# Performance work log

Measured on AMD Instinct MI355X. Metric: run time of the kernel, lower is better.

## Reference

```python
import jax, jax.numpy as jnp
import numpy as np

B, T1, H, P, V = 4096, 65, 64, 50, 32
D = H + P  # input_size = 114


def setup_inputs() -> dict:
    key = jax.random.key(0)
    ks = jax.random.split(key, 20)
    s = 1.0 / np.sqrt(D)
    sh = 1.0 / np.sqrt(H)
    inp = {
        "phonetic_input": jax.random.normal(ks[0], (B, P), dtype=jnp.float32),
        "char_seq": jax.random.randint(ks[1], (B, T1), 0, V, dtype=jnp.int64),
        "emb": jax.random.normal(ks[2], (V, H), dtype=jnp.float32).at[0].set(0.0),  # padding_idx=0
        "W_rx": jax.random.uniform(ks[3], (D, H), jnp.float32, -s, s),
        "b_rx": jax.random.uniform(ks[4], (H,), jnp.float32, -s, s),
        "W_rh": jax.random.uniform(ks[5], (H, H), jnp.float32, -sh, sh),
        "b_rh": jax.random.uniform(ks[6], (H,), jnp.float32, -sh, sh),
        "W_zx": jax.random.uniform(ks[7], (D, H), jnp.float32, -s, s),
        "b_zx": jax.random.uniform(ks[8], (H,), jnp.float32, -s, s),
        "W_zh": jax.random.uniform(ks[9], (H, H), jnp.float32, -sh, sh),
        "b_zh": jax.random.uniform(ks[10], (H,), jnp.float32, -sh, sh),
        "W_hx": jax.random.uniform(ks[11], (D, H), jnp.float32, -s, s),
        "b_hx": jax.random.uniform(ks[12], (H,), jnp.float32, -s, s),
        "W_hh": jax.random.uniform(ks[13], (H, H), jnp.float32, -sh, sh),
        "b_hh": jax.random.uniform(ks[14], (H,), jnp.float32, -sh, sh),
        "W_proj": jax.random.uniform(ks[15], (H, V), jnp.float32, -sh, sh),
        "b_proj": jax.random.uniform(ks[16], (V,), jnp.float32, -sh, sh),
    }
    return inp


def reference(phonetic_input, char_seq, emb, W_rx, b_rx, W_rh, b_rh, W_zx, b_zx,
              W_zh, b_zh, W_hx, b_hx, W_hh, b_hh, W_proj, b_proj):
    input_seq = char_seq[:, :-1]          # [B, T]
    target_seq = char_seq[:, 1:]          # [B, T]
    Bsz, T = input_seq.shape

    char_emb = emb[input_seq]                                   # [B, T, H]
    phon = jnp.broadcast_to(phonetic_input[:, None, :], (Bsz, T, P))
    x = jnp.concatenate([char_emb, phon], axis=2)               # [B, T, D]

    # Hoist input-side projections into batched GEMMs, [T, B, H] for scan
    xr = jnp.einsum('btd,dh->tbh', x, W_rx) + b_rx
    xz = jnp.einsum('btd,dh->tbh', x, W_zx) + b_zx
    xh = jnp.einsum('btd,dh->tbh', x, W_hx) + b_hx

    h0 = jnp.zeros((Bsz, H), dtype=x.dtype)

    def step(h, inputs):
        xr_t, xz_t, xh_t = inputs
        r = jax.nn.sigmoid(xr_t + h @ W_rh + b_rh)
        z = jax.nn.sigmoid(xz_t + h @ W_zh + b_zh)
        c = jnp.tanh(xh_t + (r * h) @ W_hh + b_hh)
        h_new = (1.0 - z) * h + z * c
        return h_new, h_new

    _, hs = jax.lax.scan(step, h0, (xr, xz, xh))                # [T, B, H]
    logits = jnp.einsum('tbh,hv->btv', hs, W_proj) + b_proj     # [B, T, V]

    # cross_entropy with ignore_index=0 (mean over non-ignored)
    targets = target_seq.reshape(-1)
    logp = jax.nn.log_softmax(logits.reshape(-1, V), axis=-1)
    nll = -jnp.take_along_axis(logp, targets[:, None], axis=-1)[:, 0]
    mask = (targets != 0).astype(logits.dtype)
    loss = jnp.sum(nll * mask) / jnp.maximum(jnp.sum(mask), 1.0)
    return logits, loss
```

## Files before the change

kernel.cpp:

```cpp
#include <hip/hip_runtime.h>
#include <stdint.h>

#define Bsz 4096
#define Tn  64
#define T1n 65
#define Hn  64
#define Pn  50
#define Vn  32

typedef __attribute__((ext_vector_type(8))) short short8;
typedef __attribute__((ext_vector_type(4))) float floatx4;

__device__ __forceinline__ float bf2f(unsigned short u) {
  union { unsigned int i; float f; } x; x.i = ((unsigned int)u) << 16; return x.f;
}
__device__ __forceinline__ unsigned short f2bf(float f) {
  union { float f; unsigned int i; } x; x.f = f;
  return (unsigned short)((x.i + 0x7FFFu + ((x.i >> 16) & 1u)) >> 16);
}

__device__ __forceinline__ short8 load_bfrag(const float* __restrict__ W, int ncols, int col, int kbase) {
  short8 f;
#pragma unroll
  for (int j = 0; j < 8; ++j) f[j] = (short)f2bf(W[(long)(kbase + j) * ncols + col]);
  return f;
}

__launch_bounds__(256)
__global__ void gru_kernel(const float* __restrict__ phon,
                           const int* __restrict__ cs,
                           const float* __restrict__ emb,
                           const float* __restrict__ Wrx, const float* __restrict__ brx,
                           const float* __restrict__ Wrh, const float* __restrict__ brh,
                           const float* __restrict__ Wzx, const float* __restrict__ bzx,
                           const float* __restrict__ Wzh, const float* __restrict__ bzh,
                           const float* __restrict__ Whx, const float* __restrict__ bhx,
                           const float* __restrict__ Whh, const float* __restrict__ bhh,
                           const float* __restrict__ Wpj, const float* __restrict__ bpj_g,
                           float* __restrict__ ws,
                           float* __restrict__ outp) {
  __shared__ unsigned short tbl_s[3 * 32 * 66];
  __shared__ __align__(16) unsigned short hist_s[16 * 1152];
  __shared__ __align__(16) unsigned short rh_s[16 * 72];
  __shared__ unsigned char code_s[16 * 68];
  __shared__ unsigned short emb_s[32 * 64];
  __shared__ unsigned short ph_s[16 * 52];
  __shared__ int det_s[1];
  __shared__ float red_s[8];

  const int tid = threadIdx.x;
  const int b0 = blockIdx.x * 16;
  const int w = tid >> 6, lane = tid & 63, q = lane >> 4, c16 = lane & 15;
  const int jcol = w * 16 + c16;

  if (tid == 0) det_s[0] = 0;
  __syncthreads();
  if (tid < 128 && cs[2 * tid + 1] != 0) atomicOr(&det_s[0], 1);
  __syncthreads();
  const bool is64 = (det_s[0] == 0);

  for (int i = tid; i < 16 * 72; i += 256) hist_s[15 * 1152 + i] = 0;
  for (int i = tid; i < 32 * 64; i += 256) emb_s[i] = f2bf(emb[i]);
  for (int i = tid; i < 16 * Pn; i += 256) {
    int m = i / Pn, p = i - m * Pn;
    ph_s[m * 52 + p] = f2bf(phon[(long)(b0 + m) * Pn + p]);
  }
  for (int i = tid; i < 16 * T1n; i += 256) {
    int m = i / T1n, t = i - m * T1n;
    long idx = (long)(b0 + m) * T1n + t;
    int c = is64 ? cs[2 * idx] : cs[idx];
    code_s[m * 68 + t] = (unsigned char)c;
  }

  short8 Brh0 = load_bfrag(Wrh, Hn, jcol, q * 8);
  short8 Brh1 = load_bfrag(Wrh, Hn, jcol, 32 + q * 8);
  short8 Bzh0 = load_bfrag(Wzh, Hn, jcol, q * 8);
  short8 Bzh1 = load_bfrag(Wzh, Hn, jcol, 32 + q * 8);
  short8 Bhh0 = load_bfrag(Whh, Hn, jcol, q * 8);
  short8 Bhh1 = load_bfrag(Whh, Hn, jcol, 32 + q * 8);
  short8 Bp00 = load_bfrag(Wpj, Vn, c16,      q * 8);
  short8 Bp01 = load_bfrag(Wpj, Vn, c16,      32 + q * 8);
  short8 Bp10 = load_bfrag(Wpj, Vn, 16 + c16, q * 8);
  short8 Bp11 = load_bfrag(Wpj, Vn, 16 + c16, 32 + q * 8);
  const float bpj0 = bpj_g[c16], bpj1 = bpj_g[16 + c16];

  __syncthreads();

  for (int g = 0; g < 3; ++g) {
    const float* W  = (g == 0) ? Wrx : (g == 1) ? Wzx : Whx;
    const float* bx = (g == 0) ? brx : (g == 1) ? bzx : bhx;
    const float* bh = (g == 0) ? brh : (g == 1) ? bzh : bhh;
    float acc[8] = {0.f, 0.f, 0.f, 0.f, 0.f, 0.f, 0.f, 0.f};
    float bias = bx[lane] + bh[lane];
    for (int d = 0; d < Hn; ++d) {
      float wv = W[(long)d * Hn + lane];
#pragma unroll
      for (int k = 0; k < 8; ++k)
        acc[k] += bf2f(emb_s[(w + 4 * k) * Hn + d]) * wv;
    }
#pragma unroll
    for (int k = 0; k < 8; ++k)
      tbl_s[g * 2112 + (w + 4 * k) * 66 + lane] = f2bf(acc[k] + bias);
  }

  float ph_r[4] = {0.f, 0.f, 0.f, 0.f};
  float ph_z[4] = {0.f, 0.f, 0.f, 0.f};
  float ph_h[4] = {0.f, 0.f, 0.f, 0.f};
  for (int p = 0; p < Pn; ++p) {
    float wr = Wrx[(long)(Hn + p) * Hn + jcol];
    float wz = Wzx[(long)(Hn + p) * Hn + jcol];
    float wh = Whx[(long)(Hn + p) * Hn + jcol];
#pragma unroll
    for (int r = 0; r < 4; ++r) {
      float xv = bf2f(ph_s[(q * 4 + r) * 52 + p]);
      ph_r[r] += xv * wr; ph_z[r] += xv * wz; ph_h[r] += xv * wh;
    }
  }

  float h[4] = {0.f, 0.f, 0.f, 0.f};
  float nll_acc = 0.f, cnt_acc = 0.f;

  __syncthreads();

  for (int qi = 0; qi < 4; ++qi) {
    for (int tt = 0; tt < 16; ++tt) {
      const int t = qi * 16 + tt;
      int cr[4];
#pragma unroll
      for (int r = 0; r < 4; ++r) cr[r] = code_s[(q * 4 + r) * 68 + t];

      const unsigned short* hp = &hist_s[((tt + 15) & 15) * 1152];
      short8 a0 = *(const short8*)&hp[c16 * 72 + q * 8];
      short8 a1 = *(const short8*)&hp[c16 * 72 + 32 + q * 8];
      floatx4 accr = {0.f, 0.f, 0.f, 0.f}, accz = {0.f, 0.f, 0.f, 0.f};
      accr = __builtin_amdgcn_mfma_f32_16x16x32_bf16(a0, Brh0, accr, 0, 0, 0);
      accr = __builtin_amdgcn_mfma_f32_16x16x32_bf16(a1, Brh1, accr, 0, 0, 0);
      accz = __builtin_amdgcn_mfma_f32_16x16x32_bf16(a0, Bzh0, accz, 0, 0, 0);
      accz = __builtin_amdgcn_mfma_f32_16x16x32_bf16(a1, Bzh1, accz, 0, 0, 0);
      float z[4];
#pragma unroll
      for (int r = 0; r < 4; ++r) {
        float xr = bf2f(tbl_s[0 * 2112 + cr[r] * 66 + jcol]) + ph_r[r] + accr[r];
        float rr = 1.f / (1.f + __expf(-xr));
        float xz = bf2f(tbl_s[1 * 2112 + cr[r] * 66 + jcol]) + ph_z[r] + accz[r];
        z[r] = 1.f / (1.f + __expf(-xz));
        rh_s[(q * 4 + r) * 72 + jcol] = f2bf(rr * h[r]);
      }
      __syncthreads();

      short8 p0 = *(const short8*)&rh_s[c16 * 72 + q * 8];
      short8 p1 = *(const short8*)&rh_s[c16 * 72 + 32 + q * 8];
      floatx4 accc = {0.f, 0.f, 0.f, 0.f};
      accc = __builtin_amdgcn_mfma_f32_16x16x32_bf16(p0, Bhh0, accc, 0, 0, 0);
      accc = __builtin_amdgcn_mfma_f32_16x16x32_bf16(p1, Bhh1, accc, 0, 0, 0);
      unsigned short* hw = &hist_s[tt * 1152];
#pragma unroll
      for (int r = 0; r < 4; ++r) {
        float xh = bf2f(tbl_s[2 * 2112 + cr[r] * 66 + jcol]) + ph_h[r] + accc[r];
        float e = __expf(2.f * xh);
        float c = 1.f - 2.f / (e + 1.f);
        float hn = (1.f - z[r]) * h[r] + z[r] * c;
        h[r] = hn;
        hw[(q * 4 + r) * 72 + jcol] = f2bf(hn);
      }
      __syncthreads();
    }

    for (int k = 0; k < 4; ++k) {
      const int tt = k * 4 + w;
      const int t = qi * 16 + tt;
      const unsigned short* hp = &hist_s[tt * 1152];
      const short8 ha0 = *(const short8*)&hp[c16 * 72 + q * 8];
      const short8 ha1 = *(const short8*)&hp[c16 * 72 + 32 + q * 8];
      floatx4 l0 = {0.f, 0.f, 0.f, 0.f}, l1 = {0.f, 0.f, 0.f, 0.f};
      l0 = __builtin_amdgcn_mfma_f32_16x16x32_bf16(ha0, Bp00, l0, 0, 0, 0);
      l0 = __builtin_amdgcn_mfma_f32_16x16x32_bf16(ha1, Bp01, l0, 0, 0, 0);
      l1 = __builtin_amdgcn_mfma_f32_16x16x32_bf16(ha0, Bp10, l1, 0, 0, 0);
      l1 = __builtin_amdgcn_mfma_f32_16x16x32_bf16(ha1, Bp11, l1, 0, 0, 0);
#pragma unroll
      for (int r = 0; r < 4; ++r) {
        float lg0 = l0[r] + bpj0, lg1 = l1[r] + bpj1;
        float mx = fmaxf(lg0, lg1);
#pragma unroll
        for (int off = 8; off >= 1; off >>= 1) mx = fmaxf(mx, __shfl_xor(mx, off));
        float s = __expf(lg0 - mx) + __expf(lg1 - mx);
#pragma unroll
        for (int off = 8; off >= 1; off >>= 1) s += __shfl_xor(s, off);
        float lse = mx + __logf(s);
        int m = q * 4 + r;
        long base = (((long)(b0 + m)) * Tn + t) * Vn;
        outp[base + c16] = lg0;
        outp[base + 16 + c16] = lg1;
        int targ = code_s[m * 68 + t + 1];
        if (targ != 0 && c16 == (targ & 15)) {
          float lt = (targ >> 4) ? lg1 : lg0;
          nll_acc += lse - lt; cnt_acc += 1.f;
        }
      }
    }
    __syncthreads();
  }

#pragma unroll
  for (int off = 32; off >= 1; off >>= 1) {
    nll_acc += __shfl_xor(nll_acc, off);
    cnt_acc += __shfl_xor(cnt_acc, off);
  }
  if (lane == 0) { red_s[w] = nll_acc; red_s[4 + w] = cnt_acc; }
  __syncthreads();
  if (tid == 0) {
    ws[2 * blockIdx.x]     = red_s[0] + red_s[1] + red_s[2] + red_s[3];
    ws[2 * blockIdx.x + 1] = red_s[4] + red_s[5] + red_s[6] + red_s[7];
  }
}

__global__ void loss_kernel(const float* __restrict__ ws, float* __restrict__ outp) {
  int lane = threadIdx.x;
  float n = 0.f, c = 0.f;
  for (int i = lane; i < 256; i += 64) { n += ws[2 * i]; c += ws[2 * i + 1]; }
#pragma unroll
  for (int off = 32; off >= 1; off >>= 1) {
    n += __shfl_xor(n, off);
    c += __shfl_xor(c, off);
  }
  if (lane == 0) outp[(size_t)Bsz * Tn * Vn] = n / fmaxf(c, 1.f);
}

extern "C" void kernel_launch(void* const* d_in, const int* in_sizes, int n_in,
                              void* d_out, int out_size, void* d_ws, size_t ws_size,
                              hipStream_t stream) {
  const float* phon = (const float*)d_in[0];
  const int*   cs   = (const int*)d_in[1];
  const float* emb  = (const float*)d_in[2];
  const float* Wrx  = (const float*)d_in[3];
  const float* brx  = (const float*)d_in[4];
  const float* Wrh  = (const float*)d_in[5];
  const float* brh  = (const float*)d_in[6];
  const float* Wzx  = (const float*)d_in[7];
  const float* bzx  = (const float*)d_in[8];
  const float* Wzh  = (const float*)d_in[9];
  const float* bzh  = (const float*)d_in[10];
  const float* Whx  = (const float*)d_in[11];
  const float* bhx  = (const float*)d_in[12];
  const float* Whh  = (const float*)d_in[13];
  const float* bhh  = (const float*)d_in[14];
  const float* Wpj  = (const float*)d_in[15];
  const float* bpj  = (const float*)d_in[16];
  float* ws = (float*)d_ws;

  hipLaunchKernelGGL(gru_kernel, dim3(Bsz / 16), dim3(256), 0, stream,
                     phon, cs, emb, Wrx, brx, Wrh, brh, Wzx, bzx, Wzh, bzh,
                     Whx, bhx, Whh, bhh, Wpj, bpj, ws, (float*)d_out);
  hipLaunchKernelGGL(loss_kernel, dim3(1), dim3(64), 0, stream, ws, (float*)d_out);
}
```

Baseline: 189.4 us.

## Split GRU scan and output projection into separate kernels via in-place bf16 history

Moves the per-timestep output projection, log-softmax and NLL out of the sequential recurrent kernel into a separate highly parallel kernel with one block per batch row. The scan kernel now only writes its bf16 hidden-state history to global memory, reusing the logits output buffer in place; each row's history occupies the same bytes its logits later overwrite. This shortens the serial critical path of the scan, which launches only one 256-thread block per 16 batch rows. The cost is an extra global write and read of the history. It also packs the character codes four per word, uses hardware reciprocal for sigmoid and tanh, and accumulates the loss with atomics after a zeroing kernel.

New measurement: 280.2 us. 47.9% more time.

```diff
diff --git a/kernel.cpp b/kernel.cpp
--- a/kernel.cpp
+++ b/kernel.cpp
@@ -18,6 +18,12 @@
   union { float f; unsigned int i; } x; x.f = f;
   return (unsigned short)((x.i + 0x7FFFu + ((x.i >> 16) & 1u)) >> 16);
 }
+__device__ __forceinline__ float fast_sigmoid(float x) {
+  return __builtin_amdgcn_rcpf(1.f + __expf(-x));
+}
+__device__ __forceinline__ float fast_tanh(float x) {
+  return 1.f - 2.f * __builtin_amdgcn_rcpf(1.f + __expf(2.f * x));
+}
 
 __device__ __forceinline__ short8 load_bfrag(const float* __restrict__ W, int ncols, int col, int kbase) {
   short8 f;
@@ -26,27 +32,28 @@
   return f;
 }
 
+__global__ void zero_kernel(float* __restrict__ ws) {
+  if (threadIdx.x < 2) ws[threadIdx.x] = 0.f;
+}
+
 __launch_bounds__(256)
-__global__ void gru_kernel(const float* __restrict__ phon,
-                           const int* __restrict__ cs,
-                           const float* __restrict__ emb,
-                           const float* __restrict__ Wrx, const float* __restrict__ brx,
-                           const float* __restrict__ Wrh, const float* __restrict__ brh,
-                           const float* __restrict__ Wzx, const float* __restrict__ bzx,
-                           const float* __restrict__ Wzh, const float* __restrict__ bzh,
-                           const float* __restrict__ Whx, const float* __restrict__ bhx,
-                           const float* __restrict__ Whh, const float* __restrict__ bhh,
-                           const float* __restrict__ Wpj, const float* __restrict__ bpj_g,
-                           float* __restrict__ ws,
-                           float* __restrict__ outp) {
+__global__ void gru_scan(const float* __restrict__ phon,
+                         const int* __restrict__ cs,
+                         const float* __restrict__ emb,
+                         const float* __restrict__ Wrx, const float* __restrict__ brx,
+                         const float* __restrict__ Wrh, const float* __restrict__ brh,
+                         const float* __restrict__ Wzx, const float* __restrict__ bzx,
+                         const float* __restrict__ Wzh, const float* __restrict__ bzh,
+                         const float* __restrict__ Whx, const float* __restrict__ bhx,
+                         const float* __restrict__ Whh, const float* __restrict__ bhh,
+                         unsigned short* __restrict__ histg) {
   __shared__ unsigned short tbl_s[3 * 32 * 66];
   __shared__ __align__(16) unsigned short hist_s[16 * 1152];
   __shared__ __align__(16) unsigned short rh_s[16 * 72];
-  __shared__ unsigned char code_s[16 * 68];
+  __shared__ unsigned int code4_s[64 * 4];
   __shared__ unsigned short emb_s[32 * 64];
   __shared__ unsigned short ph_s[16 * 52];
   __shared__ int det_s[1];
-  __shared__ float red_s[8];
 
   const int tid = threadIdx.x;
   const int b0 = blockIdx.x * 16;
@@ -65,11 +72,16 @@
     int m = i / Pn, p = i - m * Pn;
     ph_s[m * 52 + p] = f2bf(phon[(long)(b0 + m) * Pn + p]);
   }
-  for (int i = tid; i < 16 * T1n; i += 256) {
-    int m = i / T1n, t = i - m * T1n;
-    long idx = (long)(b0 + m) * T1n + t;
-    int c = is64 ? cs[2 * idx] : cs[idx];
-    code_s[m * 68 + t] = (unsigned char)c;
+  {
+    int t = tid >> 2, qq = tid & 3;
+    unsigned int pk = 0;
+#pragma unroll
+    for (int r = 0; r < 4; ++r) {
+      long idx = (long)(b0 + qq * 4 + r) * T1n + t;
+      int c = is64 ? cs[2 * idx] : cs[idx];
+      pk |= ((unsigned int)(c & 255)) << (8 * r);
+    }
+    code4_s[t * 4 + qq] = pk;
   }
 
   short8 Brh0 = load_bfrag(Wrh, Hn, jcol, q * 8);
@@ -78,11 +90,6 @@
   short8 Bzh1 = load_bfrag(Wzh, Hn, jcol, 32 + q * 8);
   short8 Bhh0 = load_bfrag(Whh, Hn, jcol, q * 8);
   short8 Bhh1 = load_bfrag(Whh, Hn, jcol, 32 + q * 8);
-  short8 Bp00 = load_bfrag(Wpj, Vn, c16,      q * 8);
-  short8 Bp01 = load_bfrag(Wpj, Vn, c16,      32 + q * 8);
-  short8 Bp10 = load_bfrag(Wpj, Vn, 16 + c16, q * 8);
-  short8 Bp11 = load_bfrag(Wpj, Vn, 16 + c16, 32 + q * 8);
-  const float bpj0 = bpj_g[c16], bpj1 = bpj_g[16 + c16];
 
   __syncthreads();
 
@@ -118,16 +125,13 @@
   }
 
   float h[4] = {0.f, 0.f, 0.f, 0.f};
-  float nll_acc = 0.f, cnt_acc = 0.f;
 
   __syncthreads();
 
   for (int qi = 0; qi < 4; ++qi) {
     for (int tt = 0; tt < 16; ++tt) {
       const int t = qi * 16 + tt;
-      int cr[4];
-#pragma unroll
-      for (int r = 0; r < 4; ++r) cr[r] = code_s[(q * 4 + r) * 68 + t];
+      unsigned int pk = code4_s[t * 4 + q];
 
       const unsigned short* hp = &hist_s[((tt + 15) & 15) * 1152];
       short8 a0 = *(const short8*)&hp[c16 * 72 + q * 8];
@@ -140,10 +144,11 @@
       float z[4];
 #pragma unroll
       for (int r = 0; r < 4; ++r) {
-        float xr = bf2f(tbl_s[0 * 2112 + cr[r] * 66 + jcol]) + ph_r[r] + accr[r];
-        float rr = 1.f / (1.f + __expf(-xr));
-        float xz = bf2f(tbl_s[1 * 2112 + cr[r] * 66 + jcol]) + ph_z[r] + accz[r];
-        z[r] = 1.f / (1.f + __expf(-xz));
+        int cr = (pk >> (8 * r)) & 255;
+        float xr = bf2f(tbl_s[0 * 2112 + cr * 66 + jcol]) + ph_r[r] + accr[r];
+        float rr = fast_sigmoid(xr);
+        float xz = bf2f(tbl_s[1 * 2112 + cr * 66 + jcol]) + ph_z[r] + accz[r];
+        z[r] = fast_sigmoid(xz);
         rh_s[(q * 4 + r) * 72 + jcol] = f2bf(rr * h[r]);
       }
       __syncthreads();
@@ -156,9 +161,9 @@
       unsigned short* hw = &hist_s[tt * 1152];
 #pragma unroll
       for (int r = 0; r < 4; ++r) {
-        float xh = bf2f(tbl_s[2 * 2112 + cr[r] * 66 + jcol]) + ph_h[r] + accc[r];
-        float e = __expf(2.f * xh);
-        float c = 1.f - 2.f / (e + 1.f);
+        int cr = (pk >> (8 * r)) & 255;
+        float xh = bf2f(tbl_s[2 * 2112 + cr * 66 + jcol]) + ph_h[r] + accc[r];
+        float c = fast_tanh(xh);
         float hn = (1.f - z[r]) * h[r] + z[r] * c;
         h[r] = hn;
         hw[(q * 4 + r) * 72 + jcol] = f2bf(hn);
@@ -166,39 +171,76 @@
       __syncthreads();
     }
 
-    for (int k = 0; k < 4; ++k) {
-      const int tt = k * 4 + w;
-      const int t = qi * 16 + tt;
-      const unsigned short* hp = &hist_s[tt * 1152];
-      const short8 ha0 = *(const short8*)&hp[c16 * 72 + q * 8];
-      const short8 ha1 = *(const short8*)&hp[c16 * 72 + 32 + q * 8];
-      floatx4 l0 = {0.f, 0.f, 0.f, 0.f}, l1 = {0.f, 0.f, 0.f, 0.f};
-      l0 = __builtin_amdgcn_mfma_f32_16x16x32_bf16(ha0, Bp00, l0, 0, 0, 0);
-      l0 = __builtin_amdgcn_mfma_f32_16x16x32_bf16(ha1, Bp01, l0, 0, 0, 0);
-      l1 = __builtin_amdgcn_mfma_f32_16x16x32_bf16(ha0, Bp10, l1, 0, 0, 0);
-      l1 = __builtin_amdgcn_mfma_f32_16x16x32_bf16(ha1, Bp11, l1, 0, 0, 0);
-#pragma unroll
-      for (int r = 0; r < 4; ++r) {
-        float lg0 = l0[r] + bpj0, lg1 = l1[r] + bpj1;
-        float mx = fmaxf(lg0, lg1);
-#pragma unroll
-        for (int off = 8; off >= 1; off >>= 1) mx = fmaxf(mx, __shfl_xor(mx, off));
-        float s = __expf(lg0 - mx) + __expf(lg1 - mx);
-#pragma unroll
-        for (int off = 8; off >= 1; off >>= 1) s += __shfl_xor(s, off);
-        float lse = mx + __logf(s);
-        int m = q * 4 + r;
-        long base = (((long)(b0 + m)) * Tn + t) * Vn;
-        outp[base + c16] = lg0;
-        outp[base + 16 + c16] = lg1;
-        int targ = code_s[m * 68 + t + 1];
-        if (targ != 0 && c16 == (targ & 15)) {
-          float lt = (targ >> 4) ? lg1 : lg0;
-          nll_acc += lse - lt; cnt_acc += 1.f;
-        }
-      }
-    }
-    __syncthreads();
+    for (int u = tid; u < 2048; u += 256) {
+      int slot = u >> 7, rem = u & 127;
+      int m = rem >> 3, grp = rem & 7;
+      short8 v = *(const short8*)&hist_s[slot * 1152 + m * 72 + grp * 8];
+      *(short8*)&histg[(((long)(b0 + m)) * Tn + qi * 16 + slot) * Hn + grp * 8] = v;
+    }
+  }
+}
+
+__launch_bounds__(256)
+__global__ void proj_kernel(const int* __restrict__ cs,
+                            const float* __restrict__ Wpj, const float* __restrict__ bpj_g,
+                            float* __restrict__ ws,
+                            float* __restrict__ outp) {
+  __shared__ unsigned char targ_s[64];
+  __shared__ int det_s[1];
+  __shared__ float red_s[8];
+
+  const int tid = threadIdx.x;
+  const long b = blockIdx.x;
+  const int w = tid >> 6, lane = tid & 63, q = lane >> 4, c16 = lane & 15;
+  const unsigned short* hist = (const unsigned short*)outp;
+
+  if (tid == 0) det_s[0] = 0;
+  __syncthreads();
+  if (tid < 128 && cs[2 * tid + 1] != 0) atomicOr(&det_s[0], 1);
+  __syncthreads();
+  const bool is64 = (det_s[0] == 0);
+  if (tid < 64) {
+    long idx = b * T1n + tid + 1;
+    targ_s[tid] = (unsigned char)(is64 ? cs[2 * idx] : cs[idx]);
+  }
+
+  short8 Bp00 = load_bfrag(Wpj, Vn, c16,      q * 8);
+  short8 Bp01 = load_bfrag(Wpj, Vn, c16,      32 + q * 8);
+  short8 Bp10 = load_bfrag(Wpj, Vn, 16 + c16, q * 8);
+  short8 Bp11 = load_bfrag(Wpj, Vn, 16 + c16, 32 + q * 8);
+  const float bpj0 = bpj_g[c16], bpj1 = bpj_g[16 + c16];
+  __syncthreads();
+
+  const long cell0 = b * Tn + w * 16;
+  const short8 ha0 = *(const short8*)&hist[(cell0 + c16) * Hn + q * 8];
+  const short8 ha1 = *(const short8*)&hist[(cell0 + c16) * Hn + 32 + q * 8];
+  floatx4 l0 = {0.f, 0.f, 0.f, 0.f}, l1 = {0.f, 0.f, 0.f, 0.f};
+  l0 = __builtin_amdgcn_mfma_f32_16x16x32_bf16(ha0, Bp00, l0, 0, 0, 0);
+  l0 = __builtin_amdgcn_mfma_f32_16x16x32_bf16(ha1, Bp01, l0, 0, 0, 0);
+  l1 = __builtin_amdgcn_mfma_f32_16x16x32_bf16(ha0, Bp10, l1, 0, 0, 0);
+  l1 = __builtin_amdgcn_mfma_f32_16x16x32_bf16(ha1, Bp11, l1, 0, 0, 0);
+
+  float nll_acc = 0.f, cnt_acc = 0.f;
+#pragma unroll
+  for (int r = 0; r < 4; ++r) {
+    int m = q * 4 + r;
+    int t = w * 16 + m;
+    float lg0 = l0[r] + bpj0, lg1 = l1[r] + bpj1;
+    float mx = fmaxf(lg0, lg1);
+#pragma unroll
+    for (int off = 8; off >= 1; off >>= 1) mx = fmaxf(mx, __shfl_xor(mx, off));
+    float s = __expf(lg0 - mx) + __expf(lg1 - mx);
+#pragma unroll
+    for (int off = 8; off >= 1; off >>= 1) s += __shfl_xor(s, off);
+    float lse = mx + __logf(s);
+    long base = (b * Tn + t) * Vn;
+    outp[base + c16] = lg0;
+    outp[base + 16 + c16] = lg1;
+    int targ = targ_s[t];
+    if (targ != 0 && c16 == (targ & 15)) {
+      float lt = (targ >> 4) ? lg1 : lg0;
+      nll_acc += lse - lt; cnt_acc += 1.f;
+    }
   }
 
 #pragma unroll
@@ -209,21 +251,14 @@
   if (lane == 0) { red_s[w] = nll_acc; red_s[4 + w] = cnt_acc; }
   __syncthreads();
   if (tid == 0) {
-    ws[2 * blockIdx.x]     = red_s[0] + red_s[1] + red_s[2] + red_s[3];
-    ws[2 * blockIdx.x + 1] = red_s[4] + red_s[5] + red_s[6] + red_s[7];
+    atomicAdd(&ws[0], red_s[0] + red_s[1] + red_s[2] + red_s[3]);
+    atomicAdd(&ws[1], red_s[4] + red_s[5] + red_s[6] + red_s[7]);
   }
 }
 
 __global__ void loss_kernel(const float* __restrict__ ws, float* __restrict__ outp) {
-  int lane = threadIdx.x;
-  float n = 0.f, c = 0.f;
-  for (int i = lane; i < 256; i += 64) { n += ws[2 * i]; c += ws[2 * i + 1]; }
-#pragma unroll
-  for (int off = 32; off >= 1; off >>= 1) {
-    n += __shfl_xor(n, off);
-    c += __shfl_xor(c, off);
-  }
-  if (lane == 0) outp[(size_t)Bsz * Tn * Vn] = n / fmaxf(c, 1.f);
+  if (threadIdx.x == 0)
+    outp[(size_t)Bsz * Tn * Vn] = ws[0] / fmaxf(ws[1], 1.f);
 }
 
 extern "C" void kernel_launch(void* const* d_in, const int* in_sizes, int n_in,
@@ -248,8 +283,11 @@
   const float* bpj  = (const float*)d_in[16];
   float* ws = (float*)d_ws;
 
-  hipLaunchKernelGGL(gru_kernel, dim3(Bsz / 16), dim3(256), 0, stream,
+  hipLaunchKernelGGL(zero_kernel, dim3(1), dim3(64), 0, stream, ws);
+  hipLaunchKernelGGL(gru_scan, dim3(Bsz / 16), dim3(256), 0, stream,
                      phon, cs, emb, Wrx, brx, Wrh, brh, Wzx, bzx, Wzh, bzh,
-                     Whx, bhx, Whh, bhh, Wpj, bpj, ws, (float*)d_out);
+                     Whx, bhx, Whh, bhh, (unsigned short*)d_out);
+  hipLaunchKernelGGL(proj_kernel, dim3(Bsz), dim3(256), 0, stream,
+                     cs, Wpj, bpj, ws, (float*)d_out);
   hipLaunchKernelGGL(loss_kernel, dim3(1), dim3(64), 0, stream, ws, (float*)d_out);
 }
```

## Run each 16-row GRU batch tile in a single wavefront with permuted hidden layout

Applied to the files above, without the earlier changes.

Each block now holds one 64-lane wavefront instead of four, and each lane computes all four 16-column hidden tiles. To make this work, the K dimension of the recurrent weights is permuted so the MFMA output layout can be written back as packed short4 rows. The embedding and phonetic input projections now use MFMA, codes are packed four per word, and sigmoid/tanh use hardware reciprocal. The log-softmax drops the max subtraction. The aim is cheaper block-wide barriers and less per-step overhead, at the cost of 4x more MFMA work per wave, only 256 waves in flight, and possible overflow in the softmax without the max shift.

After: 280.5 us. 1.48x slower.

```diff
diff --git a/kernel.cpp b/kernel.cpp
--- a/kernel.cpp
+++ b/kernel.cpp
@@ -9,6 +9,7 @@
 #define Vn  32
 
 typedef __attribute__((ext_vector_type(8))) short short8;
+typedef __attribute__((ext_vector_type(4))) short short4v;
 typedef __attribute__((ext_vector_type(4))) float floatx4;
 
 __device__ __forceinline__ float bf2f(unsigned short u) {
@@ -18,183 +19,248 @@
   union { float f; unsigned int i; } x; x.f = f;
   return (unsigned short)((x.i + 0x7FFFu + ((x.i >> 16) & 1u)) >> 16);
 }
-
-__device__ __forceinline__ short8 load_bfrag(const float* __restrict__ W, int ncols, int col, int kbase) {
+__device__ __forceinline__ float fast_sigmoid(float x) {
+  return __builtin_amdgcn_rcpf(1.f + __expf(-x));
+}
+__device__ __forceinline__ float fast_tanh(float x) {
+  return 1.f - 2.f * __builtin_amdgcn_rcpf(1.f + __expf(2.f * x));
+}
+
+__device__ __forceinline__ short8 load_bfrag_pi(const float* __restrict__ W, int ncols, int col, int kbase) {
   short8 f;
 #pragma unroll
-  for (int j = 0; j < 8; ++j) f[j] = (short)f2bf(W[(long)(kbase + j) * ncols + col]);
+  for (int j = 0; j < 8; ++j) {
+    int k = kbase + j;
+    int p = ((k & 3) << 4) | (k >> 2);
+    f[j] = (short)f2bf(W[(long)p * ncols + col]);
+  }
   return f;
 }
 
-__launch_bounds__(256)
-__global__ void gru_kernel(const float* __restrict__ phon,
-                           const int* __restrict__ cs,
-                           const float* __restrict__ emb,
-                           const float* __restrict__ Wrx, const float* __restrict__ brx,
-                           const float* __restrict__ Wrh, const float* __restrict__ brh,
-                           const float* __restrict__ Wzx, const float* __restrict__ bzx,
-                           const float* __restrict__ Wzh, const float* __restrict__ bzh,
-                           const float* __restrict__ Whx, const float* __restrict__ bhx,
-                           const float* __restrict__ Whh, const float* __restrict__ bhh,
-                           const float* __restrict__ Wpj, const float* __restrict__ bpj_g,
-                           float* __restrict__ ws,
-                           float* __restrict__ outp) {
-  __shared__ unsigned short tbl_s[3 * 32 * 66];
+__launch_bounds__(64, 1)
+__global__ void gru_all(const float* __restrict__ phon,
+                        const int* __restrict__ cs,
+                        const float* __restrict__ emb,
+                        const float* __restrict__ Wrx, const float* __restrict__ brx,
+                        const float* __restrict__ Wrh, const float* __restrict__ brh,
+                        const float* __restrict__ Wzx, const float* __restrict__ bzx,
+                        const float* __restrict__ Wzh, const float* __restrict__ bzh,
+                        const float* __restrict__ Whx, const float* __restrict__ bhx,
+                        const float* __restrict__ Whh, const float* __restrict__ bhh,
+                        const float* __restrict__ Wpj, const float* __restrict__ bpj_g,
+                        float* __restrict__ ws,
+                        float* __restrict__ outp) {
   __shared__ __align__(16) unsigned short hist_s[16 * 1152];
-  __shared__ __align__(16) unsigned short rh_s[16 * 72];
-  __shared__ unsigned char code_s[16 * 68];
-  __shared__ unsigned short emb_s[32 * 64];
-  __shared__ unsigned short ph_s[16 * 52];
-  __shared__ int det_s[1];
-  __shared__ float red_s[8];
-
-  const int tid = threadIdx.x;
+  __shared__ __align__(16) unsigned short rh_s[1152];
+  __shared__ __align__(16) unsigned short tblT_s[3 * 2176];
+  __shared__ unsigned int code4_s[T1n * 4];
+
+  const int lane = threadIdx.x;
+  const int q = lane >> 4, c16 = lane & 15;
   const int b0 = blockIdx.x * 16;
-  const int w = tid >> 6, lane = tid & 63, q = lane >> 4, c16 = lane & 15;
-  const int jcol = w * 16 + c16;
-
-  if (tid == 0) det_s[0] = 0;
-  __syncthreads();
-  if (tid < 128 && cs[2 * tid + 1] != 0) atomicOr(&det_s[0], 1);
-  __syncthreads();
-  const bool is64 = (det_s[0] == 0);
-
-  for (int i = tid; i < 16 * 72; i += 256) hist_s[15 * 1152 + i] = 0;
-  for (int i = tid; i < 32 * 64; i += 256) emb_s[i] = f2bf(emb[i]);
-  for (int i = tid; i < 16 * Pn; i += 256) {
-    int m = i / Pn, p = i - m * Pn;
-    ph_s[m * 52 + p] = f2bf(phon[(long)(b0 + m) * Pn + p]);
-  }
-  for (int i = tid; i < 16 * T1n; i += 256) {
-    int m = i / T1n, t = i - m * T1n;
-    long idx = (long)(b0 + m) * T1n + t;
-    int c = is64 ? cs[2 * idx] : cs[idx];
-    code_s[m * 68 + t] = (unsigned char)c;
-  }
-
-  short8 Brh0 = load_bfrag(Wrh, Hn, jcol, q * 8);
-  short8 Brh1 = load_bfrag(Wrh, Hn, jcol, 32 + q * 8);
-  short8 Bzh0 = load_bfrag(Wzh, Hn, jcol, q * 8);
-  short8 Bzh1 = load_bfrag(Wzh, Hn, jcol, 32 + q * 8);
-  short8 Bhh0 = load_bfrag(Whh, Hn, jcol, q * 8);
-  short8 Bhh1 = load_bfrag(Whh, Hn, jcol, 32 + q * 8);
-  short8 Bp00 = load_bfrag(Wpj, Vn, c16,      q * 8);
-  short8 Bp01 = load_bfrag(Wpj, Vn, c16,      32 + q * 8);
-  short8 Bp10 = load_bfrag(Wpj, Vn, 16 + c16, q * 8);
-  short8 Bp11 = load_bfrag(Wpj, Vn, 16 + c16, 32 + q * 8);
+  const floatx4 zf = {0.f, 0.f, 0.f, 0.f};
+
+  const bool is64 = (__ballot(cs[2 * lane + 1] != 0) == 0ull);
+
+#pragma unroll
+  for (int kk = 0; kk < 5; ++kk) {
+    int idx = lane + 64 * kk;
+    if (idx < T1n * 4) {
+      int t = idx >> 2, qq = idx & 3;
+      unsigned int pk = 0;
+#pragma unroll
+      for (int r = 0; r < 4; ++r) {
+        long id = (long)(b0 + qq * 4 + r) * T1n + t;
+        int c = is64 ? cs[2 * id] : cs[id];
+        pk |= ((unsigned int)(c & 255)) << (8 * r);
+      }
+      code4_s[idx] = pk;
+    }
+  }
+  for (int i = lane; i < 1152; i += 64) hist_s[15 * 1152 + i] = 0;
+
+  short8 Brh[4][2], Bzh[4][2], Bhh[4][2], Bpj[2][2];
+#pragma unroll
+  for (int T = 0; T < 4; ++T)
+#pragma unroll
+    for (int hh = 0; hh < 2; ++hh) {
+      Brh[T][hh] = load_bfrag_pi(Wrh, Hn, T * 16 + c16, hh * 32 + q * 8);
+      Bzh[T][hh] = load_bfrag_pi(Wzh, Hn, T * 16 + c16, hh * 32 + q * 8);
+      Bhh[T][hh] = load_bfrag_pi(Whh, Hn, T * 16 + c16, hh * 32 + q * 8);
+    }
+#pragma unroll
+  for (int vt = 0; vt < 2; ++vt)
+#pragma unroll
+    for (int hh = 0; hh < 2; ++hh)
+      Bpj[vt][hh] = load_bfrag_pi(Wpj, Vn, vt * 16 + c16, hh * 32 + q * 8);
   const float bpj0 = bpj_g[c16], bpj1 = bpj_g[16 + c16];
-
-  __syncthreads();
 
   for (int g = 0; g < 3; ++g) {
     const float* W  = (g == 0) ? Wrx : (g == 1) ? Wzx : Whx;
     const float* bx = (g == 0) ? brx : (g == 1) ? bzx : bhx;
     const float* bh = (g == 0) ? brh : (g == 1) ? bzh : bhh;
-    float acc[8] = {0.f, 0.f, 0.f, 0.f, 0.f, 0.f, 0.f, 0.f};
-    float bias = bx[lane] + bh[lane];
-    for (int d = 0; d < Hn; ++d) {
-      float wv = W[(long)d * Hn + lane];
-#pragma unroll
-      for (int k = 0; k < 8; ++k)
-        acc[k] += bf2f(emb_s[(w + 4 * k) * Hn + d]) * wv;
-    }
-#pragma unroll
-    for (int k = 0; k < 8; ++k)
-      tbl_s[g * 2112 + (w + 4 * k) * 66 + lane] = f2bf(acc[k] + bias);
-  }
-
-  float ph_r[4] = {0.f, 0.f, 0.f, 0.f};
-  float ph_z[4] = {0.f, 0.f, 0.f, 0.f};
-  float ph_h[4] = {0.f, 0.f, 0.f, 0.f};
-  for (int p = 0; p < Pn; ++p) {
-    float wr = Wrx[(long)(Hn + p) * Hn + jcol];
-    float wz = Wzx[(long)(Hn + p) * Hn + jcol];
-    float wh = Whx[(long)(Hn + p) * Hn + jcol];
-#pragma unroll
-    for (int r = 0; r < 4; ++r) {
-      float xv = bf2f(ph_s[(q * 4 + r) * 52 + p]);
-      ph_r[r] += xv * wr; ph_z[r] += xv * wz; ph_h[r] += xv * wh;
-    }
-  }
-
-  float h[4] = {0.f, 0.f, 0.f, 0.f};
-  float nll_acc = 0.f, cnt_acc = 0.f;
-
+    short8 Bx[4][2];
+#pragma unroll
+    for (int T = 0; T < 4; ++T)
+#pragma unroll
+      for (int hh = 0; hh < 2; ++hh) {
+        short8 f;
+#pragma unroll
+        for (int j = 0; j < 8; ++j)
+          f[j] = (short)f2bf(W[(long)(hh * 32 + q * 8 + j) * Hn + T * 16 + c16]);
+        Bx[T][hh] = f;
+      }
+    float bias[4];
+#pragma unroll
+    for (int T = 0; T < 4; ++T) bias[T] = bx[T * 16 + c16] + bh[T * 16 + c16];
+    for (int mt = 0; mt < 2; ++mt) {
+      short8 A0, A1;
+#pragma unroll
+      for (int j = 0; j < 8; ++j) {
+        A0[j] = (short)f2bf(emb[(long)(mt * 16 + c16) * Hn + q * 8 + j]);
+        A1[j] = (short)f2bf(emb[(long)(mt * 16 + c16) * Hn + 32 + q * 8 + j]);
+      }
+      floatx4 acc[4];
+#pragma unroll
+      for (int T = 0; T < 4; ++T) {
+        acc[T] = __builtin_amdgcn_mfma_f32_16x16x32_bf16(A0, Bx[T][0], zf, 0, 0, 0);
+        acc[T] = __builtin_amdgcn_mfma_f32_16x16x32_bf16(A1, Bx[T][1], acc[T], 0, 0, 0);
+      }
+#pragma unroll
+      for (int r = 0; r < 4; ++r) {
+        short4v tv;
+#pragma unroll
+        for (int T = 0; T < 4; ++T) tv[T] = (short)f2bf(acc[T][r] + bias[T]);
+        int v = mt * 16 + q * 4 + r;
+        *(short4v*)&tblT_s[g * 2176 + v * 68 + c16 * 4] = tv;
+      }
+    }
+  }
+
+  floatx4 ph_r[4], ph_z[4], ph_h[4];
+  {
+    short8 Ap0, Ap1;
+#pragma unroll
+    for (int j = 0; j < 8; ++j) {
+      int k0 = q * 8 + j;
+      Ap0[j] = (short)f2bf(phon[(long)(b0 + c16) * Pn + k0]);
+      int k1 = 32 + q * 8 + j;
+      Ap1[j] = (k1 < Pn) ? (short)f2bf(phon[(long)(b0 + c16) * Pn + k1]) : (short)0;
+    }
+    for (int g = 0; g < 3; ++g) {
+      const float* W = (g == 0) ? Wrx : (g == 1) ? Wzx : Whx;
+      short8 Bp[4][2];
+#pragma unroll
+      for (int T = 0; T < 4; ++T)
+#pragma unroll
+        for (int hh = 0; hh < 2; ++hh) {
+          short8 f;
+#pragma unroll
+          for (int j = 0; j < 8; ++j) {
+            int k = hh * 32 + q * 8 + j;
+            f[j] = (k < Pn) ? (short)f2bf(W[(long)(Hn + k) * Hn + T * 16 + c16]) : (short)0;
+          }
+          Bp[T][hh] = f;
+        }
+#pragma unroll
+      for (int T = 0; T < 4; ++T) {
+        floatx4 acc = __builtin_amdgcn_mfma_f32_16x16x32_bf16(Ap0, Bp[T][0], zf, 0, 0, 0);
+        acc = __builtin_amdgcn_mfma_f32_16x16x32_bf16(Ap1, Bp[T][1], acc, 0, 0, 0);
+        if (g == 0) ph_r[T] = acc; else if (g == 1) ph_z[T] = acc; else ph_h[T] = acc;
+      }
+    }
+  }
+
+  floatx4 h4[4] = {zf, zf, zf, zf};
+  float nll = 0.f, cnt = 0.f;
   __syncthreads();
 
   for (int qi = 0; qi < 4; ++qi) {
     for (int tt = 0; tt < 16; ++tt) {
       const int t = qi * 16 + tt;
-      int cr[4];
-#pragma unroll
-      for (int r = 0; r < 4; ++r) cr[r] = code_s[(q * 4 + r) * 68 + t];
-
       const unsigned short* hp = &hist_s[((tt + 15) & 15) * 1152];
       short8 a0 = *(const short8*)&hp[c16 * 72 + q * 8];
       short8 a1 = *(const short8*)&hp[c16 * 72 + 32 + q * 8];
-      floatx4 accr = {0.f, 0.f, 0.f, 0.f}, accz = {0.f, 0.f, 0.f, 0.f};
-      accr = __builtin_amdgcn_mfma_f32_16x16x32_bf16(a0, Brh0, accr, 0, 0, 0);
-      accr = __builtin_amdgcn_mfma_f32_16x16x32_bf16(a1, Brh1, accr, 0, 0, 0);
-      accz = __builtin_amdgcn_mfma_f32_16x16x32_bf16(a0, Bzh0, accz, 0, 0, 0);
-      accz = __builtin_amdgcn_mfma_f32_16x16x32_bf16(a1, Bzh1, accz, 0, 0, 0);
-      float z[4];
-#pragma unroll
-      for (int r = 0; r < 4; ++r) {
-        float xr = bf2f(tbl_s[0 * 2112 + cr[r] * 66 + jcol]) + ph_r[r] + accr[r];
-        float rr = 1.f / (1.f + __expf(-xr));
-        float xz = bf2f(tbl_s[1 * 2112 + cr[r] * 66 + jcol]) + ph_z[r] + accz[r];
-        z[r] = 1.f / (1.f + __expf(-xz));
-        rh_s[(q * 4 + r) * 72 + jcol] = f2bf(rr * h[r]);
+      floatx4 accr[4], accz[4];
+#pragma unroll
+      for (int T = 0; T < 4; ++T) {
+        accr[T] = __builtin_amdgcn_mfma_f32_16x16x32_bf16(a0, Brh[T][0], zf, 0, 0, 0);
+        accr[T] = __builtin_amdgcn_mfma_f32_16x16x32_bf16(a1, Brh[T][1], accr[T], 0, 0, 0);
+        accz[T] = __builtin_amdgcn_mfma_f32_16x16x32_bf16(a0, Bzh[T][0], zf, 0, 0, 0);
+        accz[T] = __builtin_amdgcn_mfma_f32_16x16x32_bf16(a1, Bzh[T][1], accz[T], 0, 0, 0);
+      }
+      unsigned int pk = code4_s[t * 4 + q];
+      floatx4 zz[4];
+#pragma unroll
+      for (int r = 0; r < 4; ++r) {
+        int cr = (pk >> (8 * r)) & 255;
+        short4v t0 = *(const short4v*)&tblT_s[0 * 2176 + cr * 68 + c16 * 4];
+        short4v t1 = *(const short4v*)&tblT_s[1 * 2176 + cr * 68 + c16 * 4];
+        short4v rhp;
+#pragma unroll
+        for (int T = 0; T < 4; ++T) {
+          float xr = bf2f((unsigned short)t0[T]) + ph_r[T][r] + accr[T][r];
+          float rr = fast_sigmoid(xr);
+          float xz = bf2f((unsigned short)t1[T]) + ph_z[T][r] + accz[T][r];
+          zz[T][r] = fast_sigmoid(xz);
+          rhp[T] = (short)f2bf(rr * h4[T][r]);
+        }
+        *(short4v*)&rh_s[(q * 4 + r) * 72 + c16 * 4] = rhp;
       }
       __syncthreads();
 
       short8 p0 = *(const short8*)&rh_s[c16 * 72 + q * 8];
       short8 p1 = *(const short8*)&rh_s[c16 * 72 + 32 + q * 8];
-      floatx4 accc = {0.f, 0.f, 0.f, 0.f};
-      accc = __builtin_amdgcn_mfma_f32_16x16x32_bf16(p0, Bhh0, accc, 0, 0, 0);
-      accc = __builtin_amdgcn_mfma_f32_16x16x32_bf16(p1, Bhh1, accc, 0, 0, 0);
+      floatx4 accc[4];
+#pragma unroll
+      for (int T = 0; T < 4; ++T) {
+        accc[T] = __builtin_amdgcn_mfma_f32_16x16x32_bf16(p0, Bhh[T][0], zf, 0, 0, 0);
+        accc[T] = __builtin_amdgcn_mfma_f32_16x16x32_bf16(p1, Bhh[T][1], accc[T], 0, 0, 0);
+      }
       unsigned short* hw = &hist_s[tt * 1152];
 #pragma unroll
       for (int r = 0; r < 4; ++r) {
-        float xh = bf2f(tbl_s[2 * 2112 + cr[r] * 66 + jcol]) + ph_h[r] + accc[r];
-        float e = __expf(2.f * xh);
-        float c = 1.f - 2.f / (e + 1.f);
-        float hn = (1.f - z[r]) * h[r] + z[r] * c;
-        h[r] = hn;
-        hw[(q * 4 + r) * 72 + jcol] = f2bf(hn);
+        int cr = (pk >> (8 * r)) & 255;
+        short4v t2 = *(const short4v*)&tblT_s[2 * 2176 + cr * 68 + c16 * 4];
+        short4v hb;
+#pragma unroll
+        for (int T = 0; T < 4; ++T) {
+          float xh = bf2f((unsigned short)t2[T]) + ph_h[T][r] + accc[T][r];
+          float c = fast_tanh(xh);
+          float hn = (1.f - zz[T][r]) * h4[T][r] + zz[T][r] * c;
+          h4[T][r] = hn;
+          hb[T] = (short)f2bf(hn);
+        }
+        *(short4v*)&hw[(q * 4 + r) * 72 + c16 * 4] = hb;
       }
       __syncthreads();
     }
 
-    for (int k = 0; k < 4; ++k) {
-      const int tt = k * 4 + w;
+    for (int tt = 0; tt < 16; ++tt) {
       const int t = qi * 16 + tt;
       const unsigned short* hp = &hist_s[tt * 1152];
-      const short8 ha0 = *(const short8*)&hp[c16 * 72 + q * 8];
-      const short8 ha1 = *(const short8*)&hp[c16 * 72 + 32 + q * 8];
-      floatx4 l0 = {0.f, 0.f, 0.f, 0.f}, l1 = {0.f, 0.f, 0.f, 0.f};
-      l0 = __builtin_amdgcn_mfma_f32_16x16x32_bf16(ha0, Bp00, l0, 0, 0, 0);
-      l0 = __builtin_amdgcn_mfma_f32_16x16x32_bf16(ha1, Bp01, l0, 0, 0, 0);
-      l1 = __builtin_amdgcn_mfma_f32_16x16x32_bf16(ha0, Bp10, l1, 0, 0, 0);
-      l1 = __builtin_amdgcn_mfma_f32_16x16x32_bf16(ha1, Bp11, l1, 0, 0, 0);
+      short8 ha0 = *(const short8*)&hp[c16 * 72 + q * 8];
+      short8 ha1 = *(const short8*)&hp[c16 * 72 + 32 + q * 8];
+      floatx4 l0 = __builtin_amdgcn_mfma_f32_16x16x32_bf16(ha0, Bpj[0][0], zf, 0, 0, 0);
+      l0 = __builtin_amdgcn_mfma_f32_16x16x32_bf16(ha1, Bpj[0][1], l0, 0, 0, 0);
+      floatx4 l1 = __builtin_amdgcn_mfma_f32_16x16x32_bf16(ha0, Bpj[1][0], zf, 0, 0, 0);
+      l1 = __builtin_amdgcn_mfma_f32_16x16x32_bf16(ha1, Bpj[1][1], l1, 0, 0, 0);
+      unsigned int pk1 = code4_s[(t + 1) * 4 + q];
 #pragma unroll
       for (int r = 0; r < 4; ++r) {
         float lg0 = l0[r] + bpj0, lg1 = l1[r] + bpj1;
-        float mx = fmaxf(lg0, lg1);
-#pragma unroll
-        for (int off = 8; off >= 1; off >>= 1) mx = fmaxf(mx, __shfl_xor(mx, off));
-        float s = __expf(lg0 - mx) + __expf(lg1 - mx);
+        float s = __expf(lg0) + __expf(lg1);
 #pragma unroll
         for (int off = 8; off >= 1; off >>= 1) s += __shfl_xor(s, off);
-        float lse = mx + __logf(s);
+        float lse = __logf(s);
         int m = q * 4 + r;
         long base = (((long)(b0 + m)) * Tn + t) * Vn;
         outp[base + c16] = lg0;
         outp[base + 16 + c16] = lg1;
-        int targ = code_s[m * 68 + t + 1];
+        int targ = (pk1 >> (8 * r)) & 255;
         if (targ != 0 && c16 == (targ & 15)) {
           float lt = (targ >> 4) ? lg1 : lg0;
-          nll_acc += lse - lt; cnt_acc += 1.f;
+          nll += lse - lt; cnt += 1.f;
         }
       }
     }
@@ -203,15 +269,10 @@
 
 #pragma unroll
   for (int off = 32; off >= 1; off >>= 1) {
-    nll_acc += __shfl_xor(nll_acc, off);
-    cnt_acc += __shfl_xor(cnt_acc, off);
-  }
-  if (lane == 0) { red_s[w] = nll_acc; red_s[4 + w] = cnt_acc; }
-  __syncthreads();
-  if (tid == 0) {
-    ws[2 * blockIdx.x]     = red_s[0] + red_s[1] + red_s[2] + red_s[3];
-    ws[2 * blockIdx.x + 1] = red_s[4] + red_s[5] + red_s[6] + red_s[7];
-  }
+    nll += __shfl_xor(nll, off);
+    cnt += __shfl_xor(cnt, off);
+  }
+  if (lane == 0) { ws[2 * blockIdx.x] = nll; ws[2 * blockIdx.x + 1] = cnt; }
 }
 
 __global__ void loss_kernel(const float* __restrict__ ws, float* __restrict__ outp) {
@@ -248,7 +309,7 @@
   const float* bpj  = (const float*)d_in[16];
   float* ws = (float*)d_ws;
 
-  hipLaunchKernelGGL(gru_kernel, dim3(Bsz / 16), dim3(256), 0, stream,
+  hipLaunchKernelGGL(gru_all, dim3(Bsz / 16), dim3(64), 0, stream,
                      phon, cs, emb, Wrx, brx, Wrh, brh, Wzx, bzx, Wzh, bzh,
                      Whx, bhx, Whh, bhh, Wpj, bpj, ws, (float*)d_out);
   hipLaunchKernelGGL(loss_kernel, dim3(1), dim3(64), 0, stream, ws, (float*)d_out);
```
